# Optimization experiments

Measured on AMD Instinct MI355X. Metric: run time of the kernel, lower is better.

The kernel has to match this reference:

```python
import jax, jax.numpy as jnp
import numpy as np

B, R, C, O, I = 256, 1152, 10, 16, 8  # batch, routes, digit caps, out dim, in dim


def conv2d(x, w, b, stride, pad):
    y = jax.lax.conv_general_dilated(
        x, w, (stride, stride), ((pad, pad), (pad, pad)),
        dimension_numbers=("NCHW", "OIHW", "NCHW"))
    return y + b[None, :, None, None]


def maxpool2(x):
    # kernel 2, stride 2, padding 1 (torch pads with -inf for max pool)
    return jax.lax.reduce_window(
        x, -jnp.inf, jax.lax.max,
        (1, 1, 2, 2), (1, 1, 2, 2), ((0, 0), (0, 0), (1, 1), (1, 1)))


def squash(t):
    sn = (t ** 2).sum(-1, keepdims=True)
    return sn * t / ((1.0 + sn) * jnp.sqrt(sn))


def setup_inputs() -> dict:
    key = jax.random.key(0)
    ks = jax.random.split(key, 8)
    return {
        "data": jax.random.normal(ks[0], (B, 3, 76, 76), dtype=jnp.float32),
        "conv1_w": jax.random.normal(ks[1], (64, 3, 3, 3), dtype=jnp.float32) * 0.1,
        "conv1_b": jnp.zeros((64,), jnp.float32),
        "conv2_w": jax.random.normal(ks[2], (128, 64, 3, 3), dtype=jnp.float32) * 0.05,
        "conv2_b": jnp.zeros((128,), jnp.float32),
        "prim_w": jax.random.normal(ks[3], (8, 32, 128, 9, 9), dtype=jnp.float32) * 0.02,
        "prim_b": jnp.zeros((8, 32), jnp.float32),
        "W": jax.random.normal(ks[4], (R, C, O, I), dtype=jnp.float32),
        "cls_w1": jax.random.normal(ks[5], (10, 160, 100), dtype=jnp.float32) * 0.05,
        "cls_b1": jnp.zeros((10, 100), jnp.float32),
        "cls_w2": jax.random.normal(ks[6], (10, 100, 1), dtype=jnp.float32) * 0.05,
        "cls_b2": jnp.zeros((10, 1), jnp.float32),
    }


def reference(data, conv1_w, conv1_b, conv2_w, conv2_b, prim_w, prim_b, W,
              cls_w1, cls_b1, cls_w2, cls_b2):
    # ---- ConvLayer ----
    x = jax.nn.relu(conv2d(data, conv1_w, conv1_b, 1, 0))   # [B,64,74,74]
    x = maxpool2(x)                                          # [B,64,38,38]
    x = jax.nn.relu(conv2d(x, conv2_w, conv2_b, 1, 1))       # [B,128,38,38]
    x = maxpool2(x)                                          # [B,128,20,20]

    # ---- PrimaryCaps: 8 parallel convs fused into one grouped-by-output conv ----
    pw = prim_w.reshape(8 * 32, 128, 9, 9)
    pb = prim_b.reshape(8 * 32)
    u = conv2d(x, pw, pb, 2, 0)                              # [B,256,6,6]
    u = u.reshape(B, R, I)                                   # [B,1152,8] (same flatten order as torch view)
    u = squash(u)

    # ---- DigitCaps dynamic routing ----
    u_hat = jnp.einsum("rcoi,bri->brco", W, u)               # [B,R,C,O]
    b_ij = jnp.zeros((R, C), u_hat.dtype)
    v_j = None
    for it in range(3):
        c_ij = jax.nn.softmax(b_ij, axis=0)                  # softmax over routes (dim=1 in torch)
        s_j = jnp.einsum("rc,brco->bco", c_ij, u_hat)        # [B,C,O]
        # torch squashes over trailing singleton dim -> elementwise squash
        v_j = squash(s_j[..., None])[..., 0]                 # [B,C,O]
        if it < 2:
            a_ij = jnp.einsum("brco,bco->brc", u_hat, v_j).mean(0)  # [R,C]
            b_ij = b_ij + a_ij

    output = v_j[..., None]                                  # [B,10,16,1]

    # ---- 10 classifiers (Linear->ReLU->Linear->Sigmoid), batched over classifier idx k ----
    feat = output.reshape(B, -1)                             # [B,160]
    h = jax.nn.relu(jnp.einsum("bf,kfh->bkh", feat, cls_w1) + cls_b1)
    logits = jnp.einsum("bkh,kho->bko", h, cls_w2) + cls_b2  # [B,10,1]
    cls = jax.nn.sigmoid(logits)[..., 0]                     # [B,10]
    return (output, cls)
```

## Files before the change

kernel.cpp:

```cpp
#include <hip/hip_runtime.h>
#include <hip/hip_bf16.h>


typedef __bf16 bf16x8 __attribute__((ext_vector_type(8)));
typedef float  f32x4  __attribute__((ext_vector_type(4)));
typedef ushort u16x8  __attribute__((ext_vector_type(8)));

static __device__ __forceinline__ ushort f2bf(float f) {
    __hip_bfloat16 h = __float2bfloat16(f);
    return *(ushort*)&h;
}
static __device__ __forceinline__ float b2f(ushort u) {
    return __uint_as_float(((unsigned)u) << 16);
}

__global__ __launch_bounds__(256) void k_prep_all(
    const float* __restrict__ w1, const float* __restrict__ w2,
    const float* __restrict__ pw, const float* __restrict__ W,
    __hip_bfloat16* __restrict__ Aw1, __hip_bfloat16* __restrict__ Aw2,
    __hip_bfloat16* __restrict__ Awt, __hip_bfloat16* __restrict__ Wt)
{
    int t = blockIdx.x * 256 + threadIdx.x;
    if (t < 2654208) {
        int oc = t / 10368, rem = t % 10368;
        int k81 = rem >> 7, ic = rem & 127;
        Awt[t] = __float2bfloat16(pw[(oc * 128 + ic) * 81 + k81]);
    } else if (t < 4128768) {
        int q = t - 2654208;
        int k = q / 160, co = q % 160;
        int r = k >> 3, i = k & 7, c = co >> 4, o = co & 15;
        Wt[q] = __float2bfloat16(W[(((size_t)r * 10 + c) * 16 + o) * 8 + i]);
    } else if (t < 4202496) {
        int q = t - 4128768;
        int oc = q / 576, rem = q % 576;
        int k9 = rem >> 6, ic = rem & 63;
        Aw2[q] = __float2bfloat16(w2[(oc * 64 + ic) * 9 + k9]);
    } else {
        int q = t - 4202496;
        int oc = q >> 5, k = q & 31;
        Aw1[q] = __float2bfloat16(k < 27 ? w1[oc * 27 + k] : 0.f);
    }
}

__global__ __launch_bounds__(256) void k_conv1_mfma(
    const float* __restrict__ data, const __hip_bfloat16* __restrict__ Aw1,
    const float* __restrict__ b1, __hip_bfloat16* __restrict__ P1t)
{
    __shared__ float tile[960];
    const int tid = threadIdx.x;
    const int py = blockIdx.x % 38, b = blockIdx.x / 38;

    #pragma unroll
    for (int c = 0; c < 4; c++) {
        int idx = tid + c * 256;
        if (idx < 960) {
            float val = 0.f;
            if (idx < 936) {
                int ic = idx / 312, rem = idx % 312;
                int rl = rem / 78, lc = rem % 78;
                int ri = 2 * py - 1 + rl, xi = lc - 1;
                if ((unsigned)ri < 76u && (unsigned)xi < 76u)
                    val = data[(b * 3 + ic) * 5776 + ri * 76 + xi];
            }
            tile[idx] = val;
        }
    }

    const int wave = tid >> 6, lane = tid & 63;
    const int l15 = lane & 15, quad = lane >> 4;

    bf16x8 af = *(const bf16x8*)((const ushort*)Aw1 + (wave * 16 + l15) * 32 + quad * 8);

    int koff[8]; bool kok[8];
    #pragma unroll
    for (int j = 0; j < 8; j++) {
        int kk = quad * 8 + j;
        kok[j] = kk < 27;
        int ic = kk / 9, rem = kk - ic * 9, ky = rem / 3, kx = rem - ky * 3;
        koff[j] = kok[j] ? (ic * 312 + ky * 78 + kx) : 0;
    }

    float bias[4];
    #pragma unroll
    for (int r = 0; r < 4; r++) bias[r] = b1[wave * 16 + quad * 4 + r];

    const bool valid0 = (py > 0);
    const bool valid1 = (py < 37);

    __syncthreads();

    #pragma unroll
    for (int t5 = 0; t5 < 5; t5++) {
        int n_x = t5 * 16 + l15;
        bool col_ok = (unsigned)(n_x - 1) < 74u;

        bf16x8 bf0, bf1;
        #pragma unroll
        for (int j = 0; j < 8; j++) {
            float v0 = tile[koff[j] + n_x];
            float v1 = tile[koff[j] + 78 + n_x];
            bool ok = col_ok && kok[j];
            bf0[j] = (__bf16)(ok ? v0 : 0.f);
            bf1[j] = (__bf16)(ok ? v1 : 0.f);
        }
        f32x4 z = {0.f, 0.f, 0.f, 0.f};
        f32x4 c0 = __builtin_amdgcn_mfma_f32_16x16x32_bf16(af, bf0, z, 0, 0, 0);
        f32x4 c1 = __builtin_amdgcn_mfma_f32_16x16x32_bf16(af, bf1, z, 0, 0, 0);

        f32x4 p;
        #pragma unroll
        for (int r = 0; r < 4; r++) {
            float r0 = (valid0 && col_ok) ? fmaxf(c0[r] + bias[r], 0.f) : 0.f;
            float r1 = (valid1 && col_ok) ? fmaxf(c1[r] + bias[r], 0.f) : 0.f;
            p[r] = fmaxf(r0, r1);
        }
        #pragma unroll
        for (int r = 0; r < 4; r++)
            p[r] = fmaxf(p[r], __shfl_xor(p[r], 1));

        if (!(l15 & 1)) {
            int px = t5 * 8 + (l15 >> 1);
            if (px < 38) {
                ushort4 pk;
                pk.x = f2bf(p[0]); pk.y = f2bf(p[1]);
                pk.z = f2bf(p[2]); pk.w = f2bf(p[3]);
                *(ushort4*)((ushort*)P1t + ((size_t)(b * 38 + py) * 38 + px) * 64
                            + wave * 16 + quad * 4) = pk;
            }
        }
    }
}

__global__ __launch_bounds__(512) void k_conv2_pool_mfma(
    const __hip_bfloat16* __restrict__ P1t,
    const __hip_bfloat16* __restrict__ Aw2,
    const float* __restrict__ cb,
    __hip_bfloat16* __restrict__ P2t)
{
    __shared__ ushort lA[128 * 72];
    __shared__ ushort lB[256 * 72];
    const int tid  = threadIdx.x;
    const int grp  = blockIdx.x / 25, toff = blockIdx.x % 25;
    const int wave = tid >> 6, lane = tid & 63;
    const int wm   = wave & 1, wn = wave >> 1;
    const int lane15 = lane & 15, quad = lane >> 4;

    const int arow = tid >> 2, apart = tid & 3;
    const int brow = tid >> 1, bpart = tid & 1;

    int off = toff * 256 + brow;
    int bb = off / 1600, rem = off % 1600;
    int cell = rem >> 2, q = rem & 3;
    int py = cell / 20, px = cell % 20;
    int y = 2 * py - 1 + (q >> 1), x = 2 * px - 1 + (q & 1);
    int b = grp * 4 + bb;

    const __hip_bfloat16* Abase = Aw2 + arow * 576;
    ushort* lAw = &lA[arow * 72 + apart * 16];
    ushort* lBw = &lB[brow * 72 + bpart * 32];
    const ushort* aRd = &lA[(wm * 64 + lane15) * 72 + quad * 8];
    const ushort* bRd = &lB[(wn * 64 + lane15) * 72 + quad * 8];

    f32x4 zero = {0.f, 0.f, 0.f, 0.f};
    f32x4 acc[4][4];
    #pragma unroll
    for (int i = 0; i < 4; i++)
        #pragma unroll
        for (int j = 0; j < 4; j++) acc[i][j] = zero;

    for (int kb = 0; kb < 9; kb++) {
        int ky = kb / 3, kx = kb - ky * 3;
        int iy = y + ky - 1, ix = x + kx - 1;
        bool ok = ((unsigned)iy < 38u) && ((unsigned)ix < 38u);

        const uint4* ga = (const uint4*)(Abase + kb * 64 + apart * 16);
        uint4 av0 = ga[0], av1 = ga[1];
        uint4 z4 = {0u, 0u, 0u, 0u};
        uint4 bv0 = z4, bv1 = z4, bv2 = z4, bv3 = z4;
        if (ok) {
            const uint4* gb = (const uint4*)(P1t + (((b * 38 + iy) * 38 + ix) << 6) + bpart * 32);
            bv0 = gb[0]; bv1 = gb[1]; bv2 = gb[2]; bv3 = gb[3];
        }

        __syncthreads();
        ((uint4*)lAw)[0] = av0; ((uint4*)lAw)[1] = av1;
        ((uint4*)lBw)[0] = bv0; ((uint4*)lBw)[1] = bv1;
        ((uint4*)lBw)[2] = bv2; ((uint4*)lBw)[3] = bv3;
        __syncthreads();

        #pragma unroll
        for (int kk = 0; kk < 2; kk++) {
            bf16x8 af[4], bf[4];
            #pragma unroll
            for (int tm = 0; tm < 4; tm++)
                af[tm] = *(const bf16x8*)(aRd + tm * 16 * 72 + kk * 32);
            #pragma unroll
            for (int tn = 0; tn < 4; tn++)
                bf[tn] = *(const bf16x8*)(bRd + tn * 16 * 72 + kk * 32);
            #pragma unroll
            for (int tm = 0; tm < 4; tm++)
                #pragma unroll
                for (int tn = 0; tn < 4; tn++)
                    acc[tm][tn] = __builtin_amdgcn_mfma_f32_16x16x32_bf16(
                        af[tm], bf[tn], acc[tm][tn], 0, 0, 0);
        }
    }

    #pragma unroll
    for (int tn = 0; tn < 4; tn++) {
        int woff = toff * 256 + wn * 64 + tn * 16 + lane15;
        int ebb = woff / 1600, erem = woff % 1600;
        int ecell = erem >> 2, eq = erem & 3;
        int epy = ecell / 20, epx = ecell % 20;
        int ey = 2 * epy - 1 + (eq >> 1), ex = 2 * epx - 1 + (eq & 1);
        bool vq = ((unsigned)ey < 38u) && ((unsigned)ex < 38u);
        int eb = grp * 4 + ebb;
        #pragma unroll
        for (int tm = 0; tm < 4; tm++) {
            int m0 = wm * 64 + tm * 16 + quad * 4;
            f32x4 a = acc[tm][tn];
            f32x4 p;
            #pragma unroll
            for (int r = 0; r < 4; r++)
                p[r] = vq ? fmaxf(a[r] + cb[m0 + r], 0.f) : 0.f;
            #pragma unroll
            for (int r = 0; r < 4; r++) {
                p[r] = fmaxf(p[r], __shfl_xor(p[r], 1));
                p[r] = fmaxf(p[r], __shfl_xor(p[r], 2));
            }
            if (eq == 0) {
                ushort4 pk;
                pk.x = f2bf(p[0]); pk.y = f2bf(p[1]);
                pk.z = f2bf(p[2]); pk.w = f2bf(p[3]);
                *(ushort4*)((ushort*)P2t + (((size_t)eb * 20 + epy) * 20 + epx) * 128 + m0) = pk;
            }
        }
    }
}

__global__ __launch_bounds__(512) void k_primcaps_mfma(
    const __hip_bfloat16* __restrict__ P2t,
    const __hip_bfloat16* __restrict__ Awt,
    float* __restrict__ partU)
{
    __shared__ ushort lA[128 * 72];
    __shared__ ushort lB[256 * 72];
    const int tid  = threadIdx.x;
    const int chunk = blockIdx.x / 72;
    const int tile  = blockIdx.x % 72;
    const int bm   = tile & 1;
    const int bn   = tile >> 1;
    const int wave = tid >> 6, lane = tid & 63;
    const int wm   = wave & 1, wn = wave >> 1;
    const int lane15 = lane & 15, quad = lane >> 4;

    const int arow = tid >> 2, apart = tid & 3;
    const int brow = tid >> 1, bpart = tid & 1;

    int n  = bn * 256 + brow;
    int cb = n / 36, cs = n % 36;
    int cy = cs / 6, cx = cs % 6;
    const __hip_bfloat16* Bbase = P2t + ((cb * 20 + 2 * cy) * 20 + 2 * cx) * 128;
    const __hip_bfloat16* Abase = Awt + (bm * 128 + arow) * 10368;
    ushort* lAw = &lA[arow * 72 + apart * 16];
    ushort* lBw = &lB[brow * 72 + bpart * 32];
    const ushort* aRd = &lA[(wm * 64 + lane15) * 72 + quad * 8];
    const ushort* bRd = &lB[(wn * 64 + lane15) * 72 + quad * 8];

    f32x4 zero = {0.f, 0.f, 0.f, 0.f};
    f32x4 acc[4][4];
    #pragma unroll
    for (int i = 0; i < 4; i++)
        #pragma unroll
        for (int j = 0; j < 4; j++) acc[i][j] = zero;

    const int kb0 = chunk * 27;
    for (int ki = 0; ki < 27; ki++) {
        int kb = kb0 + ki;
        int k81 = kb >> 1;
        int ky = k81 / 9, kx = k81 - ky * 9;
        int goffA = kb * 64 + apart * 16;
        int goffB = (ky * 20 + kx) * 128 + (kb & 1) * 64 + bpart * 32;

        const uint4* ga = (const uint4*)(Abase + goffA);
        const uint4* gb = (const uint4*)(Bbase + goffB);
        uint4 av0 = ga[0], av1 = ga[1];
        uint4 bv0 = gb[0], bv1 = gb[1], bv2 = gb[2], bv3 = gb[3];

        __syncthreads();
        ((uint4*)lAw)[0] = av0; ((uint4*)lAw)[1] = av1;
        ((uint4*)lBw)[0] = bv0; ((uint4*)lBw)[1] = bv1;
        ((uint4*)lBw)[2] = bv2; ((uint4*)lBw)[3] = bv3;
        __syncthreads();

        #pragma unroll
        for (int kk = 0; kk < 2; kk++) {
            bf16x8 af[4], bf[4];
            #pragma unroll
            for (int tm = 0; tm < 4; tm++)
                af[tm] = *(const bf16x8*)(aRd + tm * 16 * 72 + kk * 32);
            #pragma unroll
            for (int tn = 0; tn < 4; tn++)
                bf[tn] = *(const bf16x8*)(bRd + tn * 16 * 72 + kk * 32);
            #pragma unroll
            for (int tm = 0; tm < 4; tm++)
                #pragma unroll
                for (int tn = 0; tn < 4; tn++)
                    acc[tm][tn] = __builtin_amdgcn_mfma_f32_16x16x32_bf16(
                        af[tm], bf[tn], acc[tm][tn], 0, 0, 0);
        }
    }

    float* base = partU + chunk * 2359296;
    #pragma unroll
    for (int tm = 0; tm < 4; tm++) {
        int m0 = bm * 128 + wm * 64 + tm * 16 + quad * 4;
        #pragma unroll
        for (int tn = 0; tn < 4; tn++) {
            int nn = bn * 256 + wn * 64 + tn * 16 + lane15;
            int ob = nn / 36, os = nn % 36;
            float* up = base + ob * 9216 + os;
            f32x4 a = acc[tm][tn];
            #pragma unroll
            for (int r = 0; r < 4; r++)
                up[(m0 + r) * 36] = a[r];
        }
    }
}

__global__ __launch_bounds__(256) void k_reduce_squash(
    const float* __restrict__ partU, const float* __restrict__ pb,
    ushort* __restrict__ u_bf)
{
    int t = blockIdx.x * 256 + threadIdx.x;
    float4 a = {0.f, 0.f, 0.f, 0.f}, b4 = {0.f, 0.f, 0.f, 0.f};
    #pragma unroll
    for (int p = 0; p < 6; p++) {
        const float4* pp = (const float4*)(partU + p * 2359296 + t * 8);
        float4 x = pp[0], y = pp[1];
        a.x += x.x; a.y += x.y; a.z += x.z; a.w += x.w;
        b4.x += y.x; b4.y += y.y; b4.z += y.z; b4.w += y.w;
    }
    int lb = (t % 1152) * 8;
    int oc0 = lb / 36, s0 = lb - oc0 * 36;
    float vals[8] = {a.x, a.y, a.z, a.w, b4.x, b4.y, b4.z, b4.w};
    float sn = 0.f;
    #pragma unroll
    for (int e = 0; e < 8; e++) {
        int oc = oc0 + ((s0 + e) >= 36 ? 1 : 0);
        vals[e] += pb[oc];
        sn += vals[e] * vals[e];
    }
    float sc = sqrtf(sn) / (1.f + sn);
    u16x8 o8;
    #pragma unroll
    for (int e = 0; e < 8; e++) o8[e] = f2bf(vals[e] * sc);
    *(u16x8*)(u_bf + (size_t)t * 8) = o8;
}

__global__ __launch_bounds__(320) void k_sj_fused(
    const ushort* __restrict__ u_bf,
    const __hip_bfloat16* __restrict__ Wt,
    const float* __restrict__ expb,
    float* __restrict__ partS,
    int iter)
{
    __shared__ ushort ush[8 * 1152];
    __shared__ float cf[1440];
    __shared__ float sred[320];
    __shared__ float sinv[10];
    const int tid = threadIdx.x;
    const int bt = blockIdx.x & 31, kc = blockIdx.x >> 5;
    const int co = tid % 160, half = tid / 160;

    if (iter > 0) {
        int c = tid % 10, g = tid / 10;
        float s = 0.f;
        for (int r = g; r < 1152; r += 32) s += expb[r * 10 + c];
        sred[tid] = s;
        for (int i = tid; i < 1440; i += 320) cf[i] = expb[kc * 1440 + i];
        __syncthreads();
        if (tid < 10) {
            float t2 = 0.f;
            #pragma unroll
            for (int gg = 0; gg < 32; gg++) t2 += sred[tid + gg * 10];
            sinv[tid] = 1.f / t2;
        }
    }
    for (int i = tid; i < 1152; i += 320)
        ((uint4*)ush)[i] = ((const uint4*)u_bf)[(size_t)(bt * 8 + (i / 144)) * 1152
                                                + kc * 144 + (i % 144)];
    __syncthreads();

    const int cc = co >> 4;
    const float scl = (iter > 0) ? sinv[cc] : 0.f;
    const float cuni = 1.f / 1152.f;
    const ushort* wp = (const ushort*)Wt + ((size_t)kc * 1152 + half * 576) * 160 + co;

    float acc[8] = {0.f, 0.f, 0.f, 0.f, 0.f, 0.f, 0.f, 0.f};
    for (int rr = 0; rr < 72; rr++) {
        float cl = (iter == 0) ? cuni : cf[(half * 72 + rr) * 10 + cc] * scl;
        float wv[8];
        #pragma unroll
        for (int ii = 0; ii < 8; ii++)
            wv[ii] = b2f(wp[(rr * 8 + ii) * 160]) * cl;
        int kbase = half * 576 + rr * 8;
        #pragma unroll
        for (int bb = 0; bb < 8; bb++) {
            u16x8 uq = *(const u16x8*)&ush[bb * 1152 + kbase];
            #pragma unroll
            for (int ii = 0; ii < 8; ii++)
                acc[bb] += wv[ii] * b2f(uq[ii]);
        }
    }
    float* ps = partS + (kc * 2 + half) * 40960;
    #pragma unroll
    for (int bb = 0; bb < 8; bb++)
        ps[(bt * 8 + bb) * 160 + co] = acc[bb];
}

__global__ __launch_bounds__(320) void k_vj_cls(
    const float* __restrict__ partS, float* __restrict__ v,
    const float* __restrict__ w1, const float* __restrict__ b1,
    const float* __restrict__ w2, const float* __restrict__ b2,
    float* __restrict__ out, int write_out)
{
    const int b = blockIdx.x;
    const int tid = threadIdx.x;
    __shared__ float feat[160];
    if (tid < 160) {
        float s = 0.f;
        #pragma unroll
        for (int p = 0; p < 16; p++) s += partS[p * 40960 + b * 160 + tid];
        float vv = s * fabsf(s) / (1.f + s * s);
        v[b * 160 + tid] = vv;
        feat[tid] = vv;
        if (write_out) out[b * 160 + tid] = vv;
    }
    if (!write_out) return;
    __syncthreads();
    int k = tid >> 5, j = tid & 31;
    float acc = 0.f;
    for (int h = j; h < 100; h += 32) {
        float a = b1[k * 100 + h];
        for (int f = 0; f < 160; f++) a += feat[f] * w1[(k * 160 + f) * 100 + h];
        acc += fmaxf(a, 0.f) * w2[k * 100 + h];
    }
    #pragma unroll
    for (int d = 16; d > 0; d >>= 1) acc += __shfl_xor(acc, d);
    if (j == 0)
        out[40960 + b * 10 + k] = 1.f / (1.f + expf(-(acc + b2[k])));
}

__global__ __launch_bounds__(320) void k_mmat_aij(
    const ushort* __restrict__ u_bf, const float* __restrict__ v,
    const float* __restrict__ W, float* __restrict__ bij,
    float* __restrict__ expb)
{
    const int r = blockIdx.x;
    const int tid = threadIdx.x;
    const int co = tid % 160, bh = tid / 160;
    float acc[8] = {0.f, 0.f, 0.f, 0.f, 0.f, 0.f, 0.f, 0.f};
    for (int b = bh; b < 256; b += 2) {
        float vv = v[b * 160 + co];
        u16x8 uq = *(const u16x8*)(u_bf + (size_t)b * 9216 + r * 8);
        #pragma unroll
        for (int j = 0; j < 8; j++) acc[j] += vv * b2f(uq[j]);
    }
    __shared__ float red[2560];
    __shared__ float Ml[8][160];
    #pragma unroll
    for (int j = 0; j < 8; j++) red[j * 320 + bh * 160 + co] = acc[j];
    __syncthreads();
    if (tid < 160) {
        #pragma unroll
        for (int j = 0; j < 8; j++)
            Ml[j][tid] = (red[j * 320 + tid] + red[j * 320 + 160 + tid]) * (1.f / 256.f);
    }
    __syncthreads();
    int c = tid >> 5, j32 = tid & 31;
    const float* wr = W + ((size_t)r * 10 + c) * 128;
    float a2 = 0.f;
    #pragma unroll
    for (int m = 0; m < 4; m++) {
        int idx = j32 + m * 32;
        int o = idx >> 3, i = idx & 7;
        a2 += wr[idx] * Ml[i][c * 16 + o];
    }
    #pragma unroll
    for (int d = 16; d > 0; d >>= 1) a2 += __shfl_xor(a2, d);
    if (j32 == 0) {
        float nb = bij[c * 1152 + r] + a2;
        bij[c * 1152 + r] = nb;
        expb[r * 10 + c] = expf(nb);
    }
}

extern "C" void kernel_launch(void* const* d_in, const int* in_sizes, int n_in,
                              void* d_out, int out_size, void* d_ws, size_t ws_size,
                              hipStream_t stream) {
    const float* data    = (const float*)d_in[0];
    const float* conv1_w = (const float*)d_in[1];
    const float* conv1_b = (const float*)d_in[2];
    const float* conv2_w = (const float*)d_in[3];
    const float* conv2_b = (const float*)d_in[4];
    const float* prim_w  = (const float*)d_in[5];
    const float* prim_b  = (const float*)d_in[6];
    const float* W       = (const float*)d_in[7];
    const float* cls_w1  = (const float*)d_in[8];
    const float* cls_b1  = (const float*)d_in[9];
    const float* cls_w2  = (const float*)d_in[10];
    const float* cls_b2  = (const float*)d_in[11];
    float* out = (float*)d_out;

    char* ws = (char*)d_ws;
    float*          partU = (float*)(ws + 0);
    __hip_bfloat16* P2t   = (__hip_bfloat16*)(ws + 56623104);
    __hip_bfloat16* P1t   = (__hip_bfloat16*)(ws + 94633984);
    __hip_bfloat16* Awt   = (__hip_bfloat16*)(ws + 141950976);
    __hip_bfloat16* Wt    = (__hip_bfloat16*)(ws + 147259392);
    ushort*         u_bf  = (ushort*)(ws + 150208512);
    float*          partS = (float*)(ws + 154927104);
    float*          v     = (float*)(ws + 163446784);
    float*          bij   = (float*)(ws + 163610624);
    float*          expb  = (float*)(ws + 163656704);
    __hip_bfloat16* Aw2   = (__hip_bfloat16*)(ws + 163702784);
    __hip_bfloat16* Aw1   = (__hip_bfloat16*)(ws + 163850240);

    hipMemsetAsync(bij, 0, 11520 * sizeof(float), stream);

    k_prep_all<<<16424, 256, 0, stream>>>(conv1_w, conv2_w, prim_w, W,
                                          Aw1, Aw2, Awt, Wt);
    k_conv1_mfma<<<9728, 256, 0, stream>>>(data, Aw1, conv1_b, P1t);
    k_conv2_pool_mfma<<<1600, 512, 0, stream>>>(P1t, Aw2, conv2_b, P2t);
    k_primcaps_mfma<<<432, 512, 0, stream>>>(P2t, Awt, partU);
    k_reduce_squash<<<1152, 256, 0, stream>>>(partU, prim_b, u_bf);

    for (int it = 0; it < 3; it++) {
        k_sj_fused<<<256, 320, 0, stream>>>(u_bf, Wt, expb, partS, it);
        k_vj_cls<<<256, 320, 0, stream>>>(partS, v, cls_w1, cls_b1, cls_w2,
                                          cls_b2, out, it == 2 ? 1 : 0);
        if (it < 2)
            k_mmat_aij<<<1152, 320, 0, stream>>>(u_bf, v, W, bij, expb);
    }
}
```

Measured before the change: 590.5 us.

## Stage a haloed input band in LDS once for conv2 and reuse across taps

Each conv2+pool block now covers one image and a band of four pooled rows for half of the output channels. It loads a 10x42x64 haloed input patch into LDS once, then forms all nine 3x3 taps by offsetting into that patch. Before, every kernel offset reloaded its inputs from global memory and needed two barriers per step. Weights are now read straight from global/cache into registers instead of going through LDS. The cost is a large LDS footprint (about 60 KB) that limits occupancy, plus more global weight traffic per wave.

```diff
diff --git a/kernel.cpp b/kernel.cpp
--- a/kernel.cpp
+++ b/kernel.cpp
@@ -131,35 +131,47 @@
     }
 }
 
-__global__ __launch_bounds__(512) void k_conv2_pool_mfma(
+__global__ __launch_bounds__(320) void k_conv2_pool_mfma(
     const __hip_bfloat16* __restrict__ P1t,
     const __hip_bfloat16* __restrict__ Aw2,
     const float* __restrict__ cb,
     __hip_bfloat16* __restrict__ P2t)
 {
-    __shared__ ushort lA[128 * 72];
-    __shared__ ushort lB[256 * 72];
+    __shared__ ushort patch[10 * 42 * 72];
     const int tid  = threadIdx.x;
-    const int grp  = blockIdx.x / 25, toff = blockIdx.x % 25;
-    const int wave = tid >> 6, lane = tid & 63;
-    const int wm   = wave & 1, wn = wave >> 1;
-    const int lane15 = lane & 15, quad = lane >> 4;
-
-    const int arow = tid >> 2, apart = tid & 3;
-    const int brow = tid >> 1, bpart = tid & 1;
-
-    int off = toff * 256 + brow;
-    int bb = off / 1600, rem = off % 1600;
-    int cell = rem >> 2, q = rem & 3;
-    int py = cell / 20, px = cell % 20;
-    int y = 2 * py - 1 + (q >> 1), x = 2 * px - 1 + (q & 1);
-    int b = grp * 4 + bb;
-
-    const __hip_bfloat16* Abase = Aw2 + arow * 576;
-    ushort* lAw = &lA[arow * 72 + apart * 16];
-    ushort* lBw = &lB[brow * 72 + bpart * 32];
-    const ushort* aRd = &lA[(wm * 64 + lane15) * 72 + quad * 8];
-    const ushort* bRd = &lB[(wn * 64 + lane15) * 72 + quad * 8];
+    const int mh   = blockIdx.x & 1;
+    const int tblk = blockIdx.x >> 1;
+    const int band = tblk % 5, b = tblk / 5;
+    const int py0  = band * 4;
+    const int wn = tid >> 6, lane = tid & 63;
+    const int l15 = lane & 15, quad = lane >> 4;
+
+    for (int i = tid; i < 3360; i += 320) {
+        int pr = i / 336, rem = i % 336;
+        int pcol = rem >> 3, c = rem & 7;
+        int iy = 2 * py0 - 2 + pr, ix = pcol - 2;
+        uint4 val = {0u, 0u, 0u, 0u};
+        if ((unsigned)iy < 38u && (unsigned)ix < 38u)
+            val = *(const uint4*)(P1t + (((b * 38 + iy) * 38 + ix) << 6) + c * 8);
+        *(uint4*)(patch + (pr * 42 + pcol) * 72 + c * 8) = val;
+    }
+
+    int bbase[4]; bool vq[4];
+    #pragma unroll
+    for (int tn = 0; tn < 4; tn++) {
+        int n = wn * 64 + tn * 16 + l15;
+        int py_loc = n / 80, r80 = n % 80;
+        int xc = r80 >> 1, dy = n & 1;
+        bbase[tn] = (2 * py_loc + dy) * 42 + xc;
+        int cy = 2 * (py0 + py_loc) - 1 + dy;
+        int cx = xc - 1;
+        vq[tn] = ((unsigned)cy < 38u) && ((unsigned)cx < 38u);
+    }
+
+    const ushort* Arow[4];
+    #pragma unroll
+    for (int tm = 0; tm < 4; tm++)
+        Arow[tm] = (const ushort*)Aw2 + (size_t)(mh * 64 + tm * 16 + l15) * 576 + quad * 8;
 
     f32x4 zero = {0.f, 0.f, 0.f, 0.f};
     f32x4 acc[4][4];
@@ -168,71 +180,55 @@
         #pragma unroll
         for (int j = 0; j < 4; j++) acc[i][j] = zero;
 
+    __syncthreads();
+
     for (int kb = 0; kb < 9; kb++) {
         int ky = kb / 3, kx = kb - ky * 3;
-        int iy = y + ky - 1, ix = x + kx - 1;
-        bool ok = ((unsigned)iy < 38u) && ((unsigned)ix < 38u);
-
-        const uint4* ga = (const uint4*)(Abase + kb * 64 + apart * 16);
-        uint4 av0 = ga[0], av1 = ga[1];
-        uint4 z4 = {0u, 0u, 0u, 0u};
-        uint4 bv0 = z4, bv1 = z4, bv2 = z4, bv3 = z4;
-        if (ok) {
-            const uint4* gb = (const uint4*)(P1t + (((b * 38 + iy) * 38 + ix) << 6) + bpart * 32);
-            bv0 = gb[0]; bv1 = gb[1]; bv2 = gb[2]; bv3 = gb[3];
-        }
-
-        __syncthreads();
-        ((uint4*)lAw)[0] = av0; ((uint4*)lAw)[1] = av1;
-        ((uint4*)lBw)[0] = bv0; ((uint4*)lBw)[1] = bv1;
-        ((uint4*)lBw)[2] = bv2; ((uint4*)lBw)[3] = bv3;
-        __syncthreads();
-
+        int rofs = (ky * 42 + kx) * 72 + quad * 8;
+        bf16x8 af[2][4];
+        #pragma unroll
+        for (int kk = 0; kk < 2; kk++)
+            #pragma unroll
+            for (int tm = 0; tm < 4; tm++)
+                af[kk][tm] = *(const bf16x8*)(Arow[tm] + kb * 64 + kk * 32);
         #pragma unroll
         for (int kk = 0; kk < 2; kk++) {
-            bf16x8 af[4], bf[4];
-            #pragma unroll
-            for (int tm = 0; tm < 4; tm++)
-                af[tm] = *(const bf16x8*)(aRd + tm * 16 * 72 + kk * 32);
+            bf16x8 bf[4];
             #pragma unroll
             for (int tn = 0; tn < 4; tn++)
-                bf[tn] = *(const bf16x8*)(bRd + tn * 16 * 72 + kk * 32);
+                bf[tn] = *(const bf16x8*)(patch + bbase[tn] * 72 + rofs + kk * 32);
             #pragma unroll
             for (int tm = 0; tm < 4; tm++)
                 #pragma unroll
                 for (int tn = 0; tn < 4; tn++)
                     acc[tm][tn] = __builtin_amdgcn_mfma_f32_16x16x32_bf16(
-                        af[tm], bf[tn], acc[tm][tn], 0, 0, 0);
+                        af[kk][tm], bf[tn], acc[tm][tn], 0, 0, 0);
         }
     }
 
     #pragma unroll
     for (int tn = 0; tn < 4; tn++) {
-        int woff = toff * 256 + wn * 64 + tn * 16 + lane15;
-        int ebb = woff / 1600, erem = woff % 1600;
-        int ecell = erem >> 2, eq = erem & 3;
-        int epy = ecell / 20, epx = ecell % 20;
-        int ey = 2 * epy - 1 + (eq >> 1), ex = 2 * epx - 1 + (eq & 1);
-        bool vq = ((unsigned)ey < 38u) && ((unsigned)ex < 38u);
-        int eb = grp * 4 + ebb;
+        int n = wn * 64 + tn * 16 + l15;
         #pragma unroll
         for (int tm = 0; tm < 4; tm++) {
-            int m0 = wm * 64 + tm * 16 + quad * 4;
+            int m0 = mh * 64 + tm * 16 + quad * 4;
             f32x4 a = acc[tm][tn];
             f32x4 p;
             #pragma unroll
             for (int r = 0; r < 4; r++)
-                p[r] = vq ? fmaxf(a[r] + cb[m0 + r], 0.f) : 0.f;
+                p[r] = vq[tn] ? fmaxf(a[r] + cb[m0 + r], 0.f) : 0.f;
             #pragma unroll
             for (int r = 0; r < 4; r++) {
                 p[r] = fmaxf(p[r], __shfl_xor(p[r], 1));
                 p[r] = fmaxf(p[r], __shfl_xor(p[r], 2));
             }
-            if (eq == 0) {
+            if ((l15 & 3) == 0) {
+                int py = py0 + n / 80;
+                int px = (n % 80) >> 2;
                 ushort4 pk;
                 pk.x = f2bf(p[0]); pk.y = f2bf(p[1]);
                 pk.z = f2bf(p[2]); pk.w = f2bf(p[3]);
-                *(ushort4*)((ushort*)P2t + (((size_t)eb * 20 + epy) * 20 + epx) * 128 + m0) = pk;
+                *(ushort4*)((ushort*)P2t + (((size_t)b * 20 + py) * 20 + px) * 128 + m0) = pk;
             }
         }
     }
@@ -532,7 +528,7 @@
     k_prep_all<<<16424, 256, 0, stream>>>(conv1_w, conv2_w, prim_w, W,
                                           Aw1, Aw2, Awt, Wt);
     k_conv1_mfma<<<9728, 256, 0, stream>>>(data, Aw1, conv1_b, P1t);
-    k_conv2_pool_mfma<<<1600, 512, 0, stream>>>(P1t, Aw2, conv2_b, P2t);
+    k_conv2_pool_mfma<<<2560, 320, 0, stream>>>(P1t, Aw2, conv2_b, P2t);
     k_primcaps_mfma<<<432, 512, 0, stream>>>(P2t, Awt, partU);
     k_reduce_squash<<<1152, 256, 0, stream>>>(partU, prim_b, u_bf);
 
```

New measurement: 713.3 us. 20.8% more time.
